# Performance work log

Hardware: AMD Instinct MI355X
Metric: run time of the kernel (lower is better)

The kernel has to match this reference:

```python
import jax, jax.numpy as jnp
import numpy as np

KERNEL_SIZE = 6
PAD = (KERNEL_SIZE - 2) // 4  # 1


def _polyphase(k1d):
    # torch: flip(k.reshape(-1,2).permute(1,0), dims=(1,)) -> (2, K/2)
    # row 0 = even-index taps reversed, row 1 = odd-index taps reversed
    return jnp.flip(k1d.reshape(-1, 2).T, axis=1)


def _upfir_last(x, f):
    """Polyphase synthesis along last axis.
    x: (..., N), f: (2, K2). Pads reflect by PAD, correlates with each
    polyphase filter (stride-1 cross-correlation as in F.conv2d), then
    interleaves the two outputs -> (..., 2N). Even outputs come from f[0].
    """
    N = x.shape[-1]
    K2 = f.shape[1]
    pad_cfg = [(0, 0)] * (x.ndim - 1) + [(PAD, PAD)]
    xp = jnp.pad(x, pad_cfg, mode='reflect')  # (..., N + 2*PAD), N+2*PAD-K2+1 == N
    y0 = sum(f[0, j] * xp[..., j:j + N] for j in range(K2))
    y1 = sum(f[1, j] * xp[..., j:j + N] for j in range(K2))
    return jnp.stack([y0, y1], axis=-1).reshape(*x.shape[:-1], 2 * N)


def _upfir_rows(x, f):
    # synthesis along axis -2 (the H axis); matches torch's .mT transpose dance
    return jnp.swapaxes(_upfir_last(jnp.swapaxes(x, -1, -2), f), -1, -2)


def setup_inputs() -> dict:
    key = jax.random.key(0)
    ks = jax.random.split(key, 6)
    B, C, H, W = 4, 64, 256, 256
    return {
        'ss': jax.random.normal(ks[0], (B, C, H, W), dtype=jnp.float32),
        'sd': jax.random.normal(ks[1], (B, C, H, W), dtype=jnp.float32),
        'ds': jax.random.normal(ks[2], (B, C, H, W), dtype=jnp.float32),
        'dd': jax.random.normal(ks[3], (B, C, H, W), dtype=jnp.float32),
        'h': jax.random.normal(ks[4], (KERNEL_SIZE,), dtype=jnp.float32),
        'g': jax.random.normal(ks[5], (KERNEL_SIZE,), dtype=jnp.float32),
    }


def reference(ss, sd, ds, dd, h, g):
    # single level inverse 2D DWT (levels=1, normalize_approximation=False)
    fh = _polyphase(h)
    fg = _polyphase(g)
    # columns pass (along H): reconstruct low-pass rows `s` and high-pass rows `d`
    s = _upfir_rows(ss, fh) + _upfir_rows(sd, fg)  # (B,C,2H,W)
    d = _upfir_rows(ds, fh) + _upfir_rows(dd, fg)  # (B,C,2H,W)
    # rows pass (along W)
    out = _upfir_last(s, fh) + _upfir_last(d, fg)  # (B,C,2H,2W)
    return out
```

## Files before the change

kernel.cpp:

```cpp
#include <hip/hip_runtime.h>


typedef float float4v __attribute__((ext_vector_type(4)));

constexpr int Hc = 256;
constexpr int Wc = 256;

__global__ __launch_bounds__(256) void idwt_kernel(
    const float* __restrict__ ss, const float* __restrict__ sd,
    const float* __restrict__ ds, const float* __restrict__ dd,
    const float* __restrict__ hf, const float* __restrict__ gf,
    float* __restrict__ out)
{
    const int tx = threadIdx.x;
    const int ty = threadIdx.y;
    const int i  = blockIdx.x * 4 + ty;
    const int bc = blockIdx.y;

    const float h0 = hf[0], h1 = hf[1], h2 = hf[2];
    const float h3 = hf[3], h4 = hf[4], h5 = hf[5];
    const float g0 = gf[0], g1 = gf[1], g2 = gf[2];
    const float g3 = gf[3], g4 = gf[4], g5 = gf[5];

    const size_t off = (size_t)bc * (Hc * Wc);
    const float* pss = ss + off;
    const float* psd = sd + off;
    const float* pds = ds + off;
    const float* pdd = dd + off;

    const int r0 = (i == 0) ? 1 : i - 1;
    const int r1 = i;
    const int r2 = (i == Hc - 1) ? Hc - 2 : i + 1;

    const int j0 = tx * 4;
    const int cm = (j0 == 0) ? 1 : j0 - 1;
    const int cp = (j0 + 4 == Wc) ? Wc - 2 : j0 + 4;

    auto load6 = [&](const float* base, int r, float dst[6]) {
        const float* rp = base + (size_t)r * Wc;
        const float4v m = *reinterpret_cast<const float4v*>(rp + j0);
        dst[0] = rp[cm];
        dst[1] = m[0]; dst[2] = m[1];
        dst[3] = m[2]; dst[4] = m[3];
        dst[5] = rp[cp];
    };

    float vs0[6], vs1[6], vd0[6], vd1[6];
    {
        float a0[6], a1[6], a2[6], b0[6], b1[6], b2[6];
        load6(pss, r0, a0); load6(pss, r1, a1); load6(pss, r2, a2);
        load6(psd, r0, b0); load6(psd, r1, b1); load6(psd, r2, b2);
        #pragma unroll
        for (int k = 0; k < 6; ++k) {
            vs0[k] = h4*a0[k] + h2*a1[k] + h0*a2[k] + g4*b0[k] + g2*b1[k] + g0*b2[k];
            vs1[k] = h5*a0[k] + h3*a1[k] + h1*a2[k] + g5*b0[k] + g3*b1[k] + g1*b2[k];
        }
    }
    {
        float a0[6], a1[6], a2[6], b0[6], b1[6], b2[6];
        load6(pds, r0, a0); load6(pds, r1, a1); load6(pds, r2, a2);
        load6(pdd, r0, b0); load6(pdd, r1, b1); load6(pdd, r2, b2);
        #pragma unroll
        for (int k = 0; k < 6; ++k) {
            vd0[k] = h4*a0[k] + h2*a1[k] + h0*a2[k] + g4*b0[k] + g2*b1[k] + g0*b2[k];
            vd1[k] = h5*a0[k] + h3*a1[k] + h1*a2[k] + g5*b0[k] + g3*b1[k] + g1*b2[k];
        }
    }

    float o0[8], o1[8];
    #pragma unroll
    for (int t = 0; t < 4; ++t) {
        o0[2*t]   = h4*vs0[t] + h2*vs0[t+1] + h0*vs0[t+2] + g4*vd0[t] + g2*vd0[t+1] + g0*vd0[t+2];
        o0[2*t+1] = h5*vs0[t] + h3*vs0[t+1] + h1*vs0[t+2] + g5*vd0[t] + g3*vd0[t+1] + g1*vd0[t+2];
        o1[2*t]   = h4*vs1[t] + h2*vs1[t+1] + h0*vs1[t+2] + g4*vd1[t] + g2*vd1[t+1] + g0*vd1[t+2];
        o1[2*t+1] = h5*vs1[t] + h3*vs1[t+1] + h1*vs1[t+2] + g5*vd1[t] + g3*vd1[t+1] + g1*vd1[t+2];
    }

    const int W2 = 2 * Wc;
    float* orow0 = out + ((size_t)bc * (2 * Hc) + (2 * i)) * W2 + 8 * tx;
    float* orow1 = orow0 + W2;

    *reinterpret_cast<float4v*>(orow0)     = float4v{o0[0], o0[1], o0[2], o0[3]};
    *reinterpret_cast<float4v*>(orow0 + 4) = float4v{o0[4], o0[5], o0[6], o0[7]};
    *reinterpret_cast<float4v*>(orow1)     = float4v{o1[0], o1[1], o1[2], o1[3]};
    *reinterpret_cast<float4v*>(orow1 + 4) = float4v{o1[4], o1[5], o1[6], o1[7]};
}

extern "C" void kernel_launch(void* const* d_in, const int* in_sizes, int n_in,
                              void* d_out, int out_size, void* d_ws, size_t ws_size,
                              hipStream_t stream) {
    const float* ss = (const float*)d_in[0];
    const float* sd = (const float*)d_in[1];
    const float* ds = (const float*)d_in[2];
    const float* dd = (const float*)d_in[3];
    const float* hf = (const float*)d_in[4];
    const float* gf = (const float*)d_in[5];
    float* out = (float*)d_out;

    const int BC = in_sizes[0] / (Hc * Wc);
    dim3 block(64, 4);
    dim3 grid(Hc / 4, BC);
    idwt_kernel<<<grid, block, 0, stream>>>(ss, sd, ds, dd, hf, gf, out);
}
```

Before: 497.2 us.

## Stream rows per wave with register rotation and shuffle-based column halo

Each wave now processes 8 consecutive input rows, keeping the previous, current and next rows in registers so each input row is loaded roughly once instead of three times. Column halo values come from neighbouring lanes via wave shuffles instead of extra scalar global loads. This aims to cut load instructions and redundant memory traffic, at the cost of fewer blocks and a longer per-thread serial loop.

```diff
diff --git a/kernel.cpp b/kernel.cpp
--- a/kernel.cpp
+++ b/kernel.cpp
@@ -5,6 +5,8 @@
 
 constexpr int Hc = 256;
 constexpr int Wc = 256;
+constexpr int ROWS = 8;
+constexpr int WPB  = 4;
 
 __global__ __launch_bounds__(256) void idwt_kernel(
     const float* __restrict__ ss, const float* __restrict__ sd,
@@ -12,10 +14,10 @@
     const float* __restrict__ hf, const float* __restrict__ gf,
     float* __restrict__ out)
 {
-    const int tx = threadIdx.x;
-    const int ty = threadIdx.y;
-    const int i  = blockIdx.x * 4 + ty;
-    const int bc = blockIdx.y;
+    const int lane = threadIdx.x;
+    const int wid  = threadIdx.y;
+    const int i0   = (blockIdx.x * WPB + wid) * ROWS;
+    const int bc   = blockIdx.y;
 
     const float h0 = hf[0], h1 = hf[1], h2 = hf[2];
     const float h3 = hf[3], h4 = hf[4], h5 = hf[5];
@@ -23,67 +25,85 @@
     const float g3 = gf[3], g4 = gf[4], g5 = gf[5];
 
     const size_t off = (size_t)bc * (Hc * Wc);
-    const float* pss = ss + off;
-    const float* psd = sd + off;
-    const float* pds = ds + off;
-    const float* pdd = dd + off;
+    const int j0 = lane * 4;
+    const float* pss = ss + off + j0;
+    const float* psd = sd + off + j0;
+    const float* pds = ds + off + j0;
+    const float* pdd = dd + off + j0;
 
-    const int r0 = (i == 0) ? 1 : i - 1;
-    const int r1 = i;
-    const int r2 = (i == Hc - 1) ? Hc - 2 : i + 1;
-
-    const int j0 = tx * 4;
-    const int cm = (j0 == 0) ? 1 : j0 - 1;
-    const int cp = (j0 + 4 == Wc) ? Wc - 2 : j0 + 4;
-
-    auto load6 = [&](const float* base, int r, float dst[6]) {
-        const float* rp = base + (size_t)r * Wc;
-        const float4v m = *reinterpret_cast<const float4v*>(rp + j0);
-        dst[0] = rp[cm];
-        dst[1] = m[0]; dst[2] = m[1];
-        dst[3] = m[2]; dst[4] = m[3];
-        dst[5] = rp[cp];
+    auto ld = [&](const float* p, int r) -> float4v {
+        return *reinterpret_cast<const float4v*>(p + (size_t)r * Wc);
     };
 
-    float vs0[6], vs1[6], vd0[6], vd1[6];
-    {
-        float a0[6], a1[6], a2[6], b0[6], b1[6], b2[6];
-        load6(pss, r0, a0); load6(pss, r1, a1); load6(pss, r2, a2);
-        load6(psd, r0, b0); load6(psd, r1, b1); load6(psd, r2, b2);
-        #pragma unroll
-        for (int k = 0; k < 6; ++k) {
-            vs0[k] = h4*a0[k] + h2*a1[k] + h0*a2[k] + g4*b0[k] + g2*b1[k] + g0*b2[k];
-            vs1[k] = h5*a0[k] + h3*a1[k] + h1*a2[k] + g5*b0[k] + g3*b1[k] + g1*b2[k];
-        }
-    }
-    {
-        float a0[6], a1[6], a2[6], b0[6], b1[6], b2[6];
-        load6(pds, r0, a0); load6(pds, r1, a1); load6(pds, r2, a2);
-        load6(pdd, r0, b0); load6(pdd, r1, b1); load6(pdd, r2, b2);
-        #pragma unroll
-        for (int k = 0; k < 6; ++k) {
-            vd0[k] = h4*a0[k] + h2*a1[k] + h0*a2[k] + g4*b0[k] + g2*b1[k] + g0*b2[k];
-            vd1[k] = h5*a0[k] + h3*a1[k] + h1*a2[k] + g5*b0[k] + g3*b1[k] + g1*b2[k];
-        }
-    }
-
-    float o0[8], o1[8];
-    #pragma unroll
-    for (int t = 0; t < 4; ++t) {
-        o0[2*t]   = h4*vs0[t] + h2*vs0[t+1] + h0*vs0[t+2] + g4*vd0[t] + g2*vd0[t+1] + g0*vd0[t+2];
-        o0[2*t+1] = h5*vs0[t] + h3*vs0[t+1] + h1*vs0[t+2] + g5*vd0[t] + g3*vd0[t+1] + g1*vd0[t+2];
-        o1[2*t]   = h4*vs1[t] + h2*vs1[t+1] + h0*vs1[t+2] + g4*vd1[t] + g2*vd1[t+1] + g0*vd1[t+2];
-        o1[2*t+1] = h5*vs1[t] + h3*vs1[t+1] + h1*vs1[t+2] + g5*vd1[t] + g3*vd1[t+1] + g1*vd1[t+2];
-    }
+    const int rm = (i0 == 0) ? 1 : i0 - 1;
+    float4v s_m = ld(pss, rm), s_c = ld(pss, i0);
+    float4v t_m = ld(psd, rm), t_c = ld(psd, i0);
+    float4v u_m = ld(pds, rm), u_c = ld(pds, i0);
+    float4v v_m = ld(pdd, rm), v_c = ld(pdd, i0);
 
     const int W2 = 2 * Wc;
-    float* orow0 = out + ((size_t)bc * (2 * Hc) + (2 * i)) * W2 + 8 * tx;
-    float* orow1 = orow0 + W2;
+    float* obase = out + (size_t)bc * (2 * Hc) * W2 + 8 * lane;
 
-    *reinterpret_cast<float4v*>(orow0)     = float4v{o0[0], o0[1], o0[2], o0[3]};
-    *reinterpret_cast<float4v*>(orow0 + 4) = float4v{o0[4], o0[5], o0[6], o0[7]};
-    *reinterpret_cast<float4v*>(orow1)     = float4v{o1[0], o1[1], o1[2], o1[3]};
-    *reinterpret_cast<float4v*>(orow1 + 4) = float4v{o1[4], o1[5], o1[6], o1[7]};
+    auto left = [&](const float4v& w) -> float {
+        float l = __shfl_up(w[3], 1);
+        return (lane == 0) ? w[1] : l;
+    };
+    auto right = [&](const float4v& w) -> float {
+        float rr = __shfl_down(w[0], 1);
+        return (lane == 63) ? w[2] : rr;
+    };
+
+    #pragma unroll
+    for (int r = 0; r < ROWS; ++r) {
+        const int i  = i0 + r;
+        const int rn = (i + 1 < Hc) ? i + 1 : Hc - 2;
+        const float4v s_p = ld(pss, rn);
+        const float4v t_p = ld(psd, rn);
+        const float4v u_p = ld(pds, rn);
+        const float4v v_p = ld(pdd, rn);
+
+        float4v vs0, vs1, vd0, vd1;
+        #pragma unroll
+        for (int k = 0; k < 4; ++k) {
+            vs0[k] = h4*s_m[k] + h2*s_c[k] + h0*s_p[k] + g4*t_m[k] + g2*t_c[k] + g0*t_p[k];
+            vs1[k] = h5*s_m[k] + h3*s_c[k] + h1*s_p[k] + g5*t_m[k] + g3*t_c[k] + g1*t_p[k];
+            vd0[k] = h4*u_m[k] + h2*u_c[k] + h0*u_p[k] + g4*v_m[k] + g2*v_c[k] + g0*v_p[k];
+            vd1[k] = h5*u_m[k] + h3*u_c[k] + h1*u_p[k] + g5*v_m[k] + g3*v_c[k] + g1*v_p[k];
+        }
+
+        const float a [6] = { left(vs0), vs0[0], vs0[1], vs0[2], vs0[3], right(vs0) };
+        const float b [6] = { left(vd0), vd0[0], vd0[1], vd0[2], vd0[3], right(vd0) };
+        const float c2[6] = { left(vs1), vs1[0], vs1[1], vs1[2], vs1[3], right(vs1) };
+        const float d2[6] = { left(vd1), vd1[0], vd1[1], vd1[2], vd1[3], right(vd1) };
+
+        float4v o00, o01, o10, o11;
+        #pragma unroll
+        for (int t = 0; t < 4; ++t) {
+            const float e0 = h4*a [t] + h2*a [t+1] + h0*a [t+2] + g4*b [t] + g2*b [t+1] + g0*b [t+2];
+            const float e1 = h5*a [t] + h3*a [t+1] + h1*a [t+2] + g5*b [t] + g3*b [t+1] + g1*b [t+2];
+            const float f0 = h4*c2[t] + h2*c2[t+1] + h0*c2[t+2] + g4*d2[t] + g2*d2[t+1] + g0*d2[t+2];
+            const float f1 = h5*c2[t] + h3*c2[t+1] + h1*c2[t+2] + g5*d2[t] + g3*d2[t+1] + g1*d2[t+2];
+            if (t < 2) {
+                o00[2*t]   = e0; o00[2*t+1]     = e1;
+                o10[2*t]   = f0; o10[2*t+1]     = f1;
+            } else {
+                o01[2*(t-2)]   = e0; o01[2*(t-2)+1] = e1;
+                o11[2*(t-2)]   = f0; o11[2*(t-2)+1] = f1;
+            }
+        }
+
+        float* orow0 = obase + (size_t)(2 * i) * W2;
+        float* orow1 = orow0 + W2;
+        *reinterpret_cast<float4v*>(orow0)     = o00;
+        *reinterpret_cast<float4v*>(orow0 + 4) = o01;
+        *reinterpret_cast<float4v*>(orow1)     = o10;
+        *reinterpret_cast<float4v*>(orow1 + 4) = o11;
+
+        s_m = s_c; s_c = s_p;
+        t_m = t_c; t_c = t_p;
+        u_m = u_c; u_c = u_p;
+        v_m = v_c; v_c = v_p;
+    }
 }
 
 extern "C" void kernel_launch(void* const* d_in, const int* in_sizes, int n_in,
@@ -98,7 +118,7 @@
     float* out = (float*)d_out;
 
     const int BC = in_sizes[0] / (Hc * Wc);
-    dim3 block(64, 4);
-    dim3 grid(Hc / 4, BC);
+    dim3 block(64, WPB);
+    dim3 grid(Hc / (ROWS * WPB), BC);
     idwt_kernel<<<grid, block, 0, stream>>>(ss, sd, ds, dd, hf, gf, out);
 }
```

Result: faster. 452.8 us (-8.9%).
